# Performance work log

Measured on AMD Instinct MI355X. Metric: run time of the kernel, lower is better.

The kernel has to match this reference:

```python
import jax, jax.numpy as jnp
import numpy as np

B, S, D = 32, 2048, 1024

def setup_inputs() -> dict:
    key = jax.random.key(0)
    k1, k2, k3, k4, k5, k6 = jax.random.split(key, 6)
    stdv = 1.0 / np.sqrt(D)
    return {
        "hidden": jax.random.normal(k1, (B, D), dtype=jnp.float32),
        "encoder_outputs": jax.random.normal(k2, (B, S, D), dtype=jnp.float32),
        "W": jax.random.normal(k3, (2 * D, D), dtype=jnp.float32) * stdv,  # linear_out weight (x @ W)
        "b": jax.random.normal(k4, (D,), dtype=jnp.float32) * stdv,
        "v": jax.random.normal(k5, (D,), dtype=jnp.float32) * stdv,
        "src_len": jax.random.randint(k6, (B,), 1, S + 1),
    }

def reference(hidden, encoder_outputs, W, b, v, src_len):
    # hidden: [B, D]; encoder_outputs: [B, S, D]
    Bb, Ss, Dd = encoder_outputs.shape
    H = jnp.broadcast_to(hidden[:, None, :], (Bb, Ss, Dd))      # repeat over seq
    x = jnp.concatenate([H, encoder_outputs], axis=-1)           # [B, S, 2D]
    energy = jnp.tanh(x @ W + b)                                 # [B, S, D]
    scores = jnp.einsum("bsd,d->bs", energy, v)                # v . energy
    mask = jnp.arange(Ss)[None, :] >= src_len[:, None]           # True = padding
    scores = jnp.where(mask, jnp.float32(-1e18), scores)
    attn = jax.nn.softmax(scores, axis=-1)                       # [B, S]
    return attn[:, None, :]                                      # [B, 1, S]
```

## Files before the change

kernel.cpp:

```cpp
#include <hip/hip_runtime.h>
#include <stdint.h>

#define B_ 32
#define S_ 2048
#define D_ 1024

typedef __bf16 bf16x8 __attribute__((ext_vector_type(8)));
typedef float f32x4 __attribute__((ext_vector_type(4)));

__device__ __forceinline__ void gload_lds16(const void* g, void* l) {
  __builtin_amdgcn_global_load_lds(
      (const __attribute__((address_space(1))) void*)g,
      (__attribute__((address_space(3))) void*)l, 16, 0, 0);
}

__global__ void zero_ws_k(float4* p) {
  p[blockIdx.x * 256 + threadIdx.x] = make_float4(0.f, 0.f, 0.f, 0.f);
}

__global__ __launch_bounds__(256) void conv_w2_k(const float* __restrict__ W,
                                                 unsigned short* __restrict__ W2t) {
  __shared__ float t[64][65];
  int k0 = blockIdx.x * 64, n0 = blockIdx.y * 64;
  int tx = threadIdx.x & 63, ty = threadIdx.x >> 6;
#pragma unroll
  for (int i = 0; i < 16; ++i) {
    int k = i * 4 + ty;
    t[k][tx] = W[(size_t)(D_ + k0 + k) * D_ + n0 + tx];
  }
  __syncthreads();
#pragma unroll
  for (int i = 0; i < 16; ++i) {
    int n = i * 4 + ty;
    __bf16 bv = (__bf16)t[tx][n];
    W2t[(size_t)(n0 + n) * D_ + k0 + tx] = *(unsigned short*)&bv;
  }
}

__global__ __launch_bounds__(256) void conv_enc_k(const float* __restrict__ enc,
                                                  unsigned short* __restrict__ encb,
                                                  const int* __restrict__ src_len) {
  int b = blockIdx.x, c = blockIdx.y;
  int s0 = c * 32;
  if (s0 >= src_len[b]) return;
  size_t base = ((size_t)b * S_ + s0) * D_;
  const float4* src = (const float4*)(enc + base);
  bf16x8* dst = (bf16x8*)(encb + base);
#pragma unroll 4
  for (int i = threadIdx.x; i < 4096; i += 256) {
    float4 a = src[2 * i], bq = src[2 * i + 1];
    bf16x8 o;
    o[0] = (__bf16)a.x;  o[1] = (__bf16)a.y;  o[2] = (__bf16)a.z;  o[3] = (__bf16)a.w;
    o[4] = (__bf16)bq.x; o[5] = (__bf16)bq.y; o[6] = (__bf16)bq.z; o[7] = (__bf16)bq.w;
    dst[i] = o;
  }
}

__global__ __launch_bounds__(256) void compute_u_k(const float* __restrict__ hidden,
                                                   const float* __restrict__ W,
                                                   const float* __restrict__ bias,
                                                   float* __restrict__ u) {
  __shared__ float h[256];
  int b = blockIdx.x, nc = blockIdx.y, kc = blockIdx.z;
  int tid = threadIdx.x;
  h[tid] = hidden[b * D_ + kc * 256 + tid];
  __syncthreads();
  int n = nc * 256 + tid;
  float acc = 0.f;
#pragma unroll 8
  for (int k = 0; k < 256; ++k)
    acc = fmaf(h[k], W[(size_t)(kc * 256 + k) * D_ + n], acc);
  if (kc == 0) acc += bias[n];
  atomicAdd(&u[b * D_ + n], acc);
}

__global__ __launch_bounds__(256) void bahdanau_gemm2_k(
    const unsigned short* __restrict__ encb, const unsigned short* __restrict__ W2t,
    const float* __restrict__ u, const float* __restrict__ vvec,
    const int* __restrict__ src_len, float* __restrict__ scores) {
  __shared__ __align__(16) unsigned short As[128 * 64];
  __shared__ __align__(16) unsigned short Bs[128 * 64];

  int bid = blockIdx.x;
  int mlow = bid & 7;
  int rem = bid >> 3;
  int nb = rem & 7;
  int mt = (rem >> 3) * 8 + mlow;
  int m0 = mt << 7;
  int n0 = nb << 7;
  int b = m0 >> 11;
  int s0 = m0 & (S_ - 1);
  if (s0 >= src_len[b]) return;

  int tid = threadIdx.x;
  int lane = tid & 63;
  int w = tid >> 6;
  int wm = (w >> 1) << 6;
  int wn = (w & 1) << 6;

  int srow = w * 32 + (lane >> 3);
  int scol = (lane & 7) * 8;
  const unsigned short* asrc = encb + (size_t)(m0 + srow) * D_ + scol;
  const unsigned short* bsrc = W2t + (size_t)(n0 + srow) * D_ + scol;

  int lrow = lane & 15, lkc = lane >> 4;

  f32x4 acc[4][4];
  f32x4 zero = {0.f, 0.f, 0.f, 0.f};
#pragma unroll
  for (int i = 0; i < 4; ++i)
#pragma unroll
    for (int j = 0; j < 4; ++j) acc[i][j] = zero;

  for (int kt = 0; kt < 16; ++kt) {
    __syncthreads();
#pragma unroll
    for (int q = 0; q < 4; ++q) {
      gload_lds16(asrc + kt * 64 + (size_t)q * 8 * D_, As + (w * 32 + q * 8) * 64);
      gload_lds16(bsrc + kt * 64 + (size_t)q * 8 * D_, Bs + (w * 32 + q * 8) * 64);
    }
    __syncthreads();
#pragma unroll
    for (int ks = 0; ks < 2; ++ks) {
      bf16x8 af[4], bfr[4];
#pragma unroll
      for (int i = 0; i < 4; ++i)
        af[i] = *(const bf16x8*)(As + (wm + i * 16 + lrow) * 64 + ks * 32 + lkc * 8);
#pragma unroll
      for (int j = 0; j < 4; ++j)
        bfr[j] = *(const bf16x8*)(Bs + (wn + j * 16 + lrow) * 64 + ks * 32 + lkc * 8);
#pragma unroll
      for (int i = 0; i < 4; ++i)
#pragma unroll
        for (int j = 0; j < 4; ++j)
          acc[i][j] = __builtin_amdgcn_mfma_f32_16x16x32_bf16(af[i], bfr[j], acc[i][j], 0, 0, 0);
    }
  }

  float uv[4], vv[4];
#pragma unroll
  for (int j = 0; j < 4; ++j) {
    int n = n0 + wn + j * 16 + lrow;
    uv[j] = u[(b << 10) + n];
    vv[j] = vvec[n];
  }
  float part[4][4];
#pragma unroll
  for (int i = 0; i < 4; ++i)
#pragma unroll
    for (int r = 0; r < 4; ++r) part[i][r] = 0.f;
#pragma unroll
  for (int i = 0; i < 4; ++i)
#pragma unroll
    for (int j = 0; j < 4; ++j)
#pragma unroll
      for (int r = 0; r < 4; ++r) {
        float z = acc[i][j][r] + uv[j];
        float e2 = __expf(2.0f * z);
        float th = 1.0f - 2.0f * __builtin_amdgcn_rcpf(e2 + 1.0f);
        part[i][r] = fmaf(vv[j], th, part[i][r]);
      }
#pragma unroll
  for (int i = 0; i < 4; ++i)
#pragma unroll
    for (int r = 0; r < 4; ++r) {
      float s = part[i][r];
      s += __shfl_xor(s, 1, 64);
      s += __shfl_xor(s, 2, 64);
      s += __shfl_xor(s, 4, 64);
      s += __shfl_xor(s, 8, 64);
      if ((lane & 15) == 0) {
        int row = s0 + wm + i * 16 + ((lane >> 4) << 2) + r;
        atomicAdd(&scores[(b << 11) + row], s);
      }
    }
}

__global__ __launch_bounds__(256) void bahdanau_gemm_k(
    const float* __restrict__ enc, const unsigned short* __restrict__ W2t,
    const float* __restrict__ u, const float* __restrict__ vvec,
    const int* __restrict__ src_len, float* __restrict__ scores) {
  __shared__ __align__(16) unsigned short As[2][4096];
  __shared__ __align__(16) unsigned short Bs[2][4096];
  int bid = blockIdx.x;
  int mlow = bid & 7;
  int rem = bid >> 3;
  int nb = rem & 7;
  int mt = (rem >> 3) * 8 + mlow;
  int m0 = mt << 7;
  int n0 = nb << 7;
  int b = m0 >> 11;
  int s0 = m0 & (S_ - 1);
  if (s0 >= src_len[b]) return;
  int tid = threadIdx.x;
  int lane = tid & 63;
  int w = tid >> 6;
  int wm = (w >> 1) << 6;
  int wn = (w & 1) << 6;
  int arow = tid >> 1, ahalf = tid & 1;
  const float* aptr = enc + (size_t)(m0 + arow) * D_ + ahalf * 16;
  int ac0 = ((ahalf << 1) | 0) ^ (arow & 3);
  int ac1 = ((ahalf << 1) | 1) ^ (arow & 3);
  int seg0 = w << 1;
  int bn0 = (seg0 << 4) + (lane >> 2);
  int bn1 = bn0 + 16;
  int bc = (lane & 3) ^ (bn0 & 3);
  const unsigned short* bsrc0 = W2t + (size_t)(n0 + bn0) * D_ + bc * 8;
  const unsigned short* bsrc1 = W2t + (size_t)(n0 + bn1) * D_ + bc * 8;
  int lrow = lane & 15, lkc = lane >> 4;
  int fragoff = (wm + lrow) * 64 + ((lkc ^ (lrow & 3)) << 4);
  int fragoffB = (wn + lrow) * 64 + ((lkc ^ (lrow & 3)) << 4);
  float4 ar[4];
  f32x4 acc[4][4];
  f32x4 zero = {0.f, 0.f, 0.f, 0.f};
#pragma unroll
  for (int i = 0; i < 4; ++i)
#pragma unroll
    for (int j = 0; j < 4; ++j) acc[i][j] = zero;
  {
    const float4* p = (const float4*)aptr;
    ar[0] = p[0]; ar[1] = p[1]; ar[2] = p[2]; ar[3] = p[3];
    gload_lds16(bsrc0, &Bs[0][seg0 << 9]);
    gload_lds16(bsrc1, &Bs[0][(seg0 + 1) << 9]);
    bf16x8 w0, w1;
    const float* f = (const float*)ar;
#pragma unroll
    for (int j = 0; j < 8; ++j) { w0[j] = (__bf16)f[j]; w1[j] = (__bf16)f[8 + j]; }
    *(bf16x8*)((char*)As[0] + arow * 64 + (ac0 << 4)) = w0;
    *(bf16x8*)((char*)As[0] + arow * 64 + (ac1 << 4)) = w1;
  }
  __syncthreads();
  int buf = 0;
  for (int kt = 0; kt < 32; ++kt) {
    if (kt < 31) {
      const float4* p = (const float4*)(aptr + (kt + 1) * 32);
      ar[0] = p[0]; ar[1] = p[1]; ar[2] = p[2]; ar[3] = p[3];
      gload_lds16(bsrc0 + (kt + 1) * 32, &Bs[buf ^ 1][seg0 << 9]);
      gload_lds16(bsrc1 + (kt + 1) * 32, &Bs[buf ^ 1][(seg0 + 1) << 9]);
    }
    const char* ab = (const char*)As[buf] + fragoff;
    const char* bb = (const char*)Bs[buf] + fragoffB;
    bf16x8 af[4], bfr[4];
#pragma unroll
    for (int i = 0; i < 4; ++i) af[i] = *(const bf16x8*)(ab + i * 1024);
#pragma unroll
    for (int i = 0; i < 4; ++i) bfr[i] = *(const bf16x8*)(bb + i * 1024);
#pragma unroll
    for (int i = 0; i < 4; ++i)
#pragma unroll
      for (int j = 0; j < 4; ++j)
        acc[i][j] = __builtin_amdgcn_mfma_f32_16x16x32_bf16(af[i], bfr[j], acc[i][j], 0, 0, 0);
    if (kt < 31) {
      bf16x8 w0, w1;
      const float* f = (const float*)ar;
#pragma unroll
      for (int j = 0; j < 8; ++j) { w0[j] = (__bf16)f[j]; w1[j] = (__bf16)f[8 + j]; }
      *(bf16x8*)((char*)As[buf ^ 1] + arow * 64 + (ac0 << 4)) = w0;
      *(bf16x8*)((char*)As[buf ^ 1] + arow * 64 + (ac1 << 4)) = w1;
    }
    __syncthreads();
    buf ^= 1;
  }
  float uv[4], vv[4];
#pragma unroll
  for (int j = 0; j < 4; ++j) {
    int n = n0 + wn + j * 16 + lrow;
    uv[j] = u[(b << 10) + n];
    vv[j] = vvec[n];
  }
  float part[4][4];
#pragma unroll
  for (int i = 0; i < 4; ++i)
#pragma unroll
    for (int r = 0; r < 4; ++r) part[i][r] = 0.f;
#pragma unroll
  for (int i = 0; i < 4; ++i)
#pragma unroll
    for (int j = 0; j < 4; ++j)
#pragma unroll
      for (int r = 0; r < 4; ++r) {
        float z = acc[i][j][r] + uv[j];
        float e2 = __expf(2.0f * z);
        float th = 1.0f - 2.0f * __builtin_amdgcn_rcpf(e2 + 1.0f);
        part[i][r] = fmaf(vv[j], th, part[i][r]);
      }
#pragma unroll
  for (int i = 0; i < 4; ++i)
#pragma unroll
    for (int r = 0; r < 4; ++r) {
      float s = part[i][r];
      s += __shfl_xor(s, 1, 64);
      s += __shfl_xor(s, 2, 64);
      s += __shfl_xor(s, 4, 64);
      s += __shfl_xor(s, 8, 64);
      if ((lane & 15) == 0) {
        int row = s0 + wm + i * 16 + ((lane >> 4) << 2) + r;
        atomicAdd(&scores[(b << 11) + row], s);
      }
    }
}

__global__ __launch_bounds__(256) void softmax_k(const float* __restrict__ scores,
                                                 const int* __restrict__ src_len,
                                                 float* __restrict__ out) {
  __shared__ float sc[S_];
  __shared__ float red[4];
  int b = blockIdx.x;
  int L = src_len[b];
  int tid = threadIdx.x;
  const float* row = scores + b * S_;
  float mx = -3.0e38f;
  for (int s = tid; s < S_; s += 256) {
    float val = (s < L) ? row[s] : -3.0e38f;
    sc[s] = val;
    mx = fmaxf(mx, val);
  }
#pragma unroll
  for (int off = 32; off >= 1; off >>= 1) mx = fmaxf(mx, __shfl_xor(mx, off, 64));
  if ((tid & 63) == 0) red[tid >> 6] = mx;
  __syncthreads();
  mx = fmaxf(fmaxf(red[0], red[1]), fmaxf(red[2], red[3]));
  __syncthreads();
  float sum = 0.f;
  for (int s = tid; s < S_; s += 256) {
    float e = (s < L) ? __expf(sc[s] - mx) : 0.f;
    sc[s] = e;
    sum += e;
  }
#pragma unroll
  for (int off = 32; off >= 1; off >>= 1) sum += __shfl_xor(sum, off, 64);
  if ((tid & 63) == 0) red[tid >> 6] = sum;
  __syncthreads();
  sum = red[0] + red[1] + red[2] + red[3];
  float inv = 1.0f / sum;
  for (int s = tid; s < S_; s += 256) out[b * S_ + s] = sc[s] * inv;
}

extern "C" void kernel_launch(void* const* d_in, const int* in_sizes, int n_in,
                              void* d_out, int out_size, void* d_ws, size_t ws_size,
                              hipStream_t stream) {
  const float* hidden = (const float*)d_in[0];
  const float* enc = (const float*)d_in[1];
  const float* W = (const float*)d_in[2];
  const float* bias = (const float*)d_in[3];
  const float* v = (const float*)d_in[4];
  const int* src_len = (const int*)d_in[5];
  float* out = (float*)d_out;

  char* ws = (char*)d_ws;
  float* scores = (float*)ws;
  float* u = (float*)(ws + 256 * 1024);
  unsigned short* W2t = (unsigned short*)(ws + 384 * 1024);
  unsigned short* encb = (unsigned short*)(ws + 4ull * 1024 * 1024);
  const size_t need = 4ull * 1024 * 1024 + (size_t)B_ * S_ * D_ * 2;

  zero_ws_k<<<dim3(96), dim3(256), 0, stream>>>((float4*)scores);
  conv_w2_k<<<dim3(16, 16), dim3(256), 0, stream>>>(W, W2t);
  compute_u_k<<<dim3(32, 4, 4), dim3(256), 0, stream>>>(hidden, W, bias, u);
  if (ws_size >= need) {
    conv_enc_k<<<dim3(32, 64), dim3(256), 0, stream>>>(enc, encb, src_len);
    bahdanau_gemm2_k<<<dim3(4096), dim3(256), 0, stream>>>(encb, W2t, u, v, src_len, scores);
  } else {
    bahdanau_gemm_k<<<dim3(4096), dim3(256), 0, stream>>>(enc, W2t, u, v, src_len, scores);
  }
  softmax_k<<<dim3(32), dim3(256), 0, stream>>>(scores, src_len, out);
}
```

Baseline: 519.6 us.

## Replace bf16 GEMM with 256x256 tile, 4-stage pipelined, swizzled LDS kernel

```diff
diff --git a/kernel.cpp b/kernel.cpp
--- a/kernel.cpp
+++ b/kernel.cpp
@@ -60,82 +60,110 @@
                                                    const float* __restrict__ W,
                                                    const float* __restrict__ bias,
                                                    float* __restrict__ u) {
-  __shared__ float h[256];
-  int b = blockIdx.x, nc = blockIdx.y, kc = blockIdx.z;
-  int tid = threadIdx.x;
-  h[tid] = hidden[b * D_ + kc * 256 + tid];
-  __syncthreads();
-  int n = nc * 256 + tid;
-  float acc = 0.f;
+  __shared__ float h[D_];
+  int b = blockIdx.x, nc = blockIdx.y;
+  for (int i = threadIdx.x; i < D_; i += 256) h[i] = hidden[b * D_ + i];
+  __syncthreads();
+  int n = nc * 256 + threadIdx.x;
+  float acc = bias[n];
 #pragma unroll 8
-  for (int k = 0; k < 256; ++k)
-    acc = fmaf(h[k], W[(size_t)(kc * 256 + k) * D_ + n], acc);
-  if (kc == 0) acc += bias[n];
-  atomicAdd(&u[b * D_ + n], acc);
-}
-
-__global__ __launch_bounds__(256) void bahdanau_gemm2_k(
+  for (int k = 0; k < D_; ++k) acc = fmaf(h[k], W[(size_t)k * D_ + n], acc);
+  u[b * D_ + n] = acc;
+}
+
+__global__ __launch_bounds__(512, 2) void bahdanau_gemm3_k(
     const unsigned short* __restrict__ encb, const unsigned short* __restrict__ W2t,
     const float* __restrict__ u, const float* __restrict__ vvec,
     const int* __restrict__ src_len, float* __restrict__ scores) {
-  __shared__ __align__(16) unsigned short As[128 * 64];
-  __shared__ __align__(16) unsigned short Bs[128 * 64];
+  __shared__ __align__(16) unsigned short As3[4][256 * 32];
+  __shared__ __align__(16) unsigned short Bs3[4][256 * 32];
 
   int bid = blockIdx.x;
-  int mlow = bid & 7;
-  int rem = bid >> 3;
-  int nb = rem & 7;
-  int mt = (rem >> 3) * 8 + mlow;
-  int m0 = mt << 7;
-  int n0 = nb << 7;
+  int wg = (bid & 7) * 128 + (bid >> 3);
+  int mt = wg >> 2;
+  int n0 = (wg & 3) << 8;
+  int m0 = mt << 8;
   int b = m0 >> 11;
   int s0 = m0 & (S_ - 1);
-  if (s0 >= src_len[b]) return;
+  int L = src_len[b];
+  if (s0 >= L) return;
 
   int tid = threadIdx.x;
   int lane = tid & 63;
   int w = tid >> 6;
-  int wm = (w >> 1) << 6;
-  int wn = (w & 1) << 6;
-
-  int srow = w * 32 + (lane >> 3);
-  int scol = (lane & 7) * 8;
-  const unsigned short* asrc = encb + (size_t)(m0 + srow) * D_ + scol;
-  const unsigned short* bsrc = W2t + (size_t)(n0 + srow) * D_ + scol;
-
+  int wm = (w >> 2) << 7;
+  int wn = (w & 3) << 6;
   int lrow = lane & 15, lkc = lane >> 4;
-
-  f32x4 acc[4][4];
+  int kxr = (lkc ^ ((lrow >> 2) & 3)) * 8;
+
+  int srow = w * 32 + (lane >> 2);
+  int kx = (lane & 3) ^ ((srow >> 2) & 3);
+  const unsigned short* aS0 = encb + (size_t)(m0 + srow) * D_ + kx * 8;
+  const unsigned short* bS0 = W2t + (size_t)(n0 + srow) * D_ + kx * 8;
+  int dst0 = (w * 2) * 512, dst1 = (w * 2 + 1) * 512;
+
+#define STAGE3(t_) do { int sl_ = (t_) & 3; int ko_ = (t_) * 32;              \
+    gload_lds16(aS0 + ko_, &As3[sl_][dst0]);                                   \
+    gload_lds16(aS0 + 16 * D_ + ko_, &As3[sl_][dst1]);                         \
+    gload_lds16(bS0 + ko_, &Bs3[sl_][dst0]);                                   \
+    gload_lds16(bS0 + 16 * D_ + ko_, &Bs3[sl_][dst1]); } while (0)
+
+  f32x4 acc[8][4];
   f32x4 zero = {0.f, 0.f, 0.f, 0.f};
 #pragma unroll
-  for (int i = 0; i < 4; ++i)
+  for (int i = 0; i < 8; ++i)
 #pragma unroll
     for (int j = 0; j < 4; ++j) acc[i][j] = zero;
 
-  for (int kt = 0; kt < 16; ++kt) {
-    __syncthreads();
-#pragma unroll
-    for (int q = 0; q < 4; ++q) {
-      gload_lds16(asrc + kt * 64 + (size_t)q * 8 * D_, As + (w * 32 + q * 8) * 64);
-      gload_lds16(bsrc + kt * 64 + (size_t)q * 8 * D_, Bs + (w * 32 + q * 8) * 64);
-    }
-    __syncthreads();
-#pragma unroll
-    for (int ks = 0; ks < 2; ++ks) {
-      bf16x8 af[4], bfr[4];
-#pragma unroll
-      for (int i = 0; i < 4; ++i)
-        af[i] = *(const bf16x8*)(As + (wm + i * 16 + lrow) * 64 + ks * 32 + lkc * 8);
-#pragma unroll
-      for (int j = 0; j < 4; ++j)
-        bfr[j] = *(const bf16x8*)(Bs + (wn + j * 16 + lrow) * 64 + ks * 32 + lkc * 8);
-#pragma unroll
-      for (int i = 0; i < 4; ++i)
+  bool act[8];
+#pragma unroll
+  for (int i = 0; i < 8; ++i) act[i] = (s0 + wm + i * 16) < L;
+
+  STAGE3(0); STAGE3(1); STAGE3(2);
+
+  for (int t = 0; t < 32; ++t) {
+    if (t <= 29)      asm volatile("s_waitcnt vmcnt(8)" ::: "memory");
+    else if (t == 30) asm volatile("s_waitcnt vmcnt(4)" ::: "memory");
+    else              asm volatile("s_waitcnt vmcnt(0)" ::: "memory");
+    __builtin_amdgcn_s_barrier();
+    __builtin_amdgcn_sched_barrier(0);
+    const unsigned short* Aslot = As3[t & 3];
+    const unsigned short* Bslot = Bs3[t & 3];
+
+    bf16x8 af[4], bfr[4];
+#pragma unroll
+    for (int j = 0; j < 4; ++j)
+      bfr[j] = *(const bf16x8*)(Bslot + (wn + j * 16 + lrow) * 32 + kxr);
+#pragma unroll
+    for (int i = 0; i < 4; ++i)
+      af[i] = *(const bf16x8*)(Aslot + (wm + i * 16 + lrow) * 32 + kxr);
+    if (t < 29) { int tn = t + 3; int sl = tn & 3; int ko = tn * 32;
+      gload_lds16(aS0 + ko, &As3[sl][dst0]);
+      gload_lds16(aS0 + 16 * D_ + ko, &As3[sl][dst1]); }
+    __builtin_amdgcn_s_setprio(1);
+#pragma unroll
+    for (int i = 0; i < 4; ++i)
+      if (act[i])
 #pragma unroll
         for (int j = 0; j < 4; ++j)
           acc[i][j] = __builtin_amdgcn_mfma_f32_16x16x32_bf16(af[i], bfr[j], acc[i][j], 0, 0, 0);
-    }
-  }
+    __builtin_amdgcn_s_setprio(0);
+#pragma unroll
+    for (int i = 0; i < 4; ++i)
+      af[i] = *(const bf16x8*)(Aslot + (wm + (i + 4) * 16 + lrow) * 32 + kxr);
+    if (t < 29) { int tn = t + 3; int sl = tn & 3; int ko = tn * 32;
+      gload_lds16(bS0 + ko, &Bs3[sl][dst0]);
+      gload_lds16(bS0 + 16 * D_ + ko, &Bs3[sl][dst1]); }
+    __builtin_amdgcn_s_setprio(1);
+#pragma unroll
+    for (int i = 0; i < 4; ++i)
+      if (act[i + 4])
+#pragma unroll
+        for (int j = 0; j < 4; ++j)
+          acc[i + 4][j] = __builtin_amdgcn_mfma_f32_16x16x32_bf16(af[i], bfr[j], acc[i + 4][j], 0, 0, 0);
+    __builtin_amdgcn_s_setprio(0);
+  }
+#undef STAGE3
 
   float uv[4], vv[4];
 #pragma unroll
@@ -144,13 +172,12 @@
     uv[j] = u[(b << 10) + n];
     vv[j] = vvec[n];
   }
-  float part[4][4];
-#pragma unroll
-  for (int i = 0; i < 4; ++i)
-#pragma unroll
-    for (int r = 0; r < 4; ++r) part[i][r] = 0.f;
-#pragma unroll
-  for (int i = 0; i < 4; ++i)
+#pragma unroll
+  for (int i = 0; i < 8; ++i) {
+    if (!act[i]) continue;
+    float part[4];
+#pragma unroll
+    for (int r = 0; r < 4; ++r) part[r] = 0.f;
 #pragma unroll
     for (int j = 0; j < 4; ++j)
 #pragma unroll
@@ -158,22 +185,21 @@
         float z = acc[i][j][r] + uv[j];
         float e2 = __expf(2.0f * z);
         float th = 1.0f - 2.0f * __builtin_amdgcn_rcpf(e2 + 1.0f);
-        part[i][r] = fmaf(vv[j], th, part[i][r]);
+        part[r] = fmaf(vv[j], th, part[r]);
       }
 #pragma unroll
-  for (int i = 0; i < 4; ++i)
-#pragma unroll
     for (int r = 0; r < 4; ++r) {
-      float s = part[i][r];
+      float s = part[r];
       s += __shfl_xor(s, 1, 64);
       s += __shfl_xor(s, 2, 64);
       s += __shfl_xor(s, 4, 64);
       s += __shfl_xor(s, 8, 64);
       if ((lane & 15) == 0) {
-        int row = s0 + wm + i * 16 + ((lane >> 4) << 2) + r;
+        int row = s0 + wm + i * 16 + (lkc << 2) + r;
         atomicAdd(&scores[(b << 11) + row], s);
       }
     }
+  }
 }
 
 __global__ __launch_bounds__(256) void bahdanau_gemm_k(
@@ -354,12 +380,12 @@
   unsigned short* encb = (unsigned short*)(ws + 4ull * 1024 * 1024);
   const size_t need = 4ull * 1024 * 1024 + (size_t)B_ * S_ * D_ * 2;
 
-  zero_ws_k<<<dim3(96), dim3(256), 0, stream>>>((float4*)scores);
+  zero_ws_k<<<dim3(64), dim3(256), 0, stream>>>((float4*)scores);
   conv_w2_k<<<dim3(16, 16), dim3(256), 0, stream>>>(W, W2t);
-  compute_u_k<<<dim3(32, 4, 4), dim3(256), 0, stream>>>(hidden, W, bias, u);
+  compute_u_k<<<dim3(32, 4), dim3(256), 0, stream>>>(hidden, W, bias, u);
   if (ws_size >= need) {
     conv_enc_k<<<dim3(32, 64), dim3(256), 0, stream>>>(enc, encb, src_len);
-    bahdanau_gemm2_k<<<dim3(4096), dim3(256), 0, stream>>>(encb, W2t, u, v, src_len, scores);
+    bahdanau_gemm3_k<<<dim3(1024), dim3(512), 0, stream>>>(encb, W2t, u, v, src_len, scores);
   } else {
     bahdanau_gemm_k<<<dim3(4096), dim3(256), 0, stream>>>(enc, W2t, u, v, src_len, scores);
   }
```

Measured after the change: 569.4 us. 1.1x slower.
